# Optimization experiments

Hardware: AMD Instinct MI355X
Metric: run time of the kernel (lower is better)

## Reference

```python
import jax, jax.numpy as jnp
import numpy as np

# Module config (matches init_kwargs)
N_HEADS = 16
HEAD = 64
SEQ = 4096          # single prefill sequence (cu_seqlens_k = [0, SEQ])
BS = 64             # block_size (both q and k blocks)
LOCAL = 8           # local_blocks
VERT = 8            # vert_stride
NB = SEQ // BS      # number of blocks along seq
SLIDE = max(1, VERT // N_HEADS)  # get_head_sliding_step(16, 8, homo_head=False) -> 1
SM_SCALE = 1.0 / float(np.sqrt(HEAD))


def _build_layout():
    """Per-head block-sparse layout: causal + (local OR strided-vertical) blocks,
    padded to a fixed max nnz per row (CSR rows -> padded col indices + valid mask)."""
    h = np.arange(N_HEADS)[:, None, None]
    i = np.arange(NB)[None, :, None]
    j = np.arange(NB)[None, None, :]
    mask = (j <= i) & (((i - j) < LOCAL) | (((j + h * SLIDE + 1) % VERT) == 0))
    max_nnz = int(mask.sum(-1).max())
    cols = np.zeros((N_HEADS, NB, max_nnz), np.int32)
    valid = np.zeros((N_HEADS, NB, max_nnz), bool)
    for hh in range(N_HEADS):
        for ii in range(NB):
            c = np.nonzero(mask[hh, ii])[0]
            cols[hh, ii, :len(c)] = c
            valid[hh, ii, :len(c)] = True
    return cols, valid, max_nnz

_COLS_NP, _VALID_NP, MAX_NNZ = _build_layout()
COLS = jnp.asarray(_COLS_NP)    # [H, NB, NNZ] k-block ids (padded with 0)
VALID = jnp.asarray(_VALID_NP)  # [H, NB, NNZ] padding mask


def setup_inputs() -> dict:
    key = jax.random.key(0)
    kq, kk, kv = jax.random.split(key, 3)
    q = jax.random.normal(kq, (SEQ, N_HEADS, HEAD), jnp.float32)
    k = jax.random.normal(kk, (SEQ, N_HEADS, HEAD), jnp.float32)
    v = jax.random.normal(kv, (SEQ, N_HEADS, HEAD), jnp.float32)
    cu_seqlens_k = jnp.array([0, SEQ], jnp.int32)
    return {"q": q, "k": k, "v": v, "cu_seqlens_k": cu_seqlens_k}


def _attn(q, k, v):
    # [T, H, D] -> [H, NB, BS, D]
    qb = q.transpose(1, 0, 2).reshape(N_HEADS, NB, BS, HEAD)
    kb = k.transpose(1, 0, 2).reshape(N_HEADS, NB, BS, HEAD)
    vb = v.transpose(1, 0, 2).reshape(N_HEADS, NB, BS, HEAD)
    gather = jax.vmap(lambda x, c: x[c])  # per-head block gather
    kg = gather(kb, COLS)  # [H, NB, NNZ, BS, D]
    vg = gather(vb, COLS)  # [H, NB, NNZ, BS, D]
    # block-sparse scores: [H, NB(q blk), BS(m), NNZ(n), BS(j)]
    scores = jnp.einsum('himd,hinjd->himnj', qb, kg) * SM_SCALE
    qpos = jnp.arange(NB)[:, None] * BS + jnp.arange(BS)[None, :]   # [NB, BS]
    kpos = COLS[..., None] * BS + jnp.arange(BS)                    # [H, NB, NNZ, BS]
    allow = VALID[:, :, None, :, None] & (
        qpos[None, :, :, None, None] >= kpos[:, :, None, :, :])
    scores = jnp.where(allow, scores, -jnp.inf)
    p = jax.nn.softmax(scores.reshape(N_HEADS, NB, BS, MAX_NNZ * BS), axis=-1)
    p = p.reshape(N_HEADS, NB, BS, MAX_NNZ, BS)
    out = jnp.einsum('himnj,hinjd->himd', p, vg)
    return out.reshape(N_HEADS, SEQ, HEAD).transpose(1, 0, 2)  # [T, H, D]


def reference(q, k, v, cu_seqlens_k):
    # single-sequence prefill: past_len = 0, q_len == k_len == SEQ
    return _attn(q, k, v)
```

## Files before the change

kernel.cpp:

```cpp
#include <hip/hip_runtime.h>
#include <hip/hip_bf16.h>
#include <math.h>


#define NHEADS 16
#define HDIM   64
#define NBLK   64
#define SEQLEN 4096
#define KP     72
#define SMAX   16.0f

typedef __attribute__((ext_vector_type(8))) short bf16x8;
typedef __attribute__((ext_vector_type(4))) float f32x4;

__device__ __forceinline__ short f2bf(float x) {
    union { float f; unsigned u; } c; c.f = x;
    unsigned u = c.u;
    return (short)((u + 0x7FFFu + ((u >> 16) & 1u)) >> 16);
}

__device__ __forceinline__ void load_lds16(const short* g, const short* l) {
    __builtin_amdgcn_global_load_lds(
        (const __attribute__((address_space(1))) void*)g,
        (__attribute__((address_space(3))) void*)l, 16, 0, 0);
}

__global__ __launch_bounds__(256)
void prep_kernel(const float* __restrict__ k, const float* __restrict__ v,
                 short* __restrict__ kt, short* __restrict__ vt) {
    __shared__ short tile[64 * KP];
    const int b = blockIdx.x;
    const int h = b >> 6, jb = b & 63;
    const int tid = threadIdx.x;

    #pragma unroll
    for (int it = 0; it < 4; ++it) {
        int e = it * 1024 + tid * 4;
        int key = e >> 6, d0 = e & 63;
        float4 f = *(const float4*)(v + ((size_t)(jb * 64 + key) * NHEADS + h) * HDIM + d0);
        tile[(d0 + 0) * KP + key] = f2bf(f.x);
        tile[(d0 + 1) * KP + key] = f2bf(f.y);
        tile[(d0 + 2) * KP + key] = f2bf(f.z);
        tile[(d0 + 3) * KP + key] = f2bf(f.w);
    }
    __syncthreads();
    short* vtile = vt + (size_t)b * 4096;
    #pragma unroll
    for (int ii = 0; ii < 2; ++ii) {
        int idx = ii * 256 + tid;
        int d = idx >> 3, gsw = idx & 7;
        int g = gsw ^ (d & 7);
        bf16x8 val = *(const bf16x8*)&tile[d * KP + g * 8];
        *(bf16x8*)(vtile + (size_t)idx * 8) = val;
    }
    short* ktile = kt + (size_t)b * 4096;
    #pragma unroll
    for (int ii = 0; ii < 2; ++ii) {
        int idx = ii * 256 + tid;
        int r = idx >> 3, g = idx & 7;
        const float* src = k + ((size_t)(jb * 64 + r) * NHEADS + h) * HDIM + g * 8;
        float4 f0 = *(const float4*)src;
        float4 f1 = *(const float4*)(src + 4);
        bf16x8 a;
        a[0]=f2bf(f0.x); a[1]=f2bf(f0.y); a[2]=f2bf(f0.z); a[3]=f2bf(f0.w);
        a[4]=f2bf(f1.x); a[5]=f2bf(f1.y); a[6]=f2bf(f1.z); a[7]=f2bf(f1.w);
        int G = r * 8 + (g ^ (r & 7));
        *(bf16x8*)(ktile + (size_t)G * 8) = a;
    }
}

__global__ __launch_bounds__(256, 4)
void attn_kernel(const short* __restrict__ kt, const short* __restrict__ vt,
                 const float* __restrict__ q, float* __restrict__ out) {
    __shared__ short kv[8192];
    __shared__ short pl[4 * 16 * KP];

    const int b    = blockIdx.x;
    const int h    = ((b & 7) << 1) | ((b >> 3) & 1);
    const int g6   = b >> 4;
    const int qi   = (g6 & 1) ? (63 - (g6 >> 1)) : (g6 >> 1);
    const int tid  = threadIdx.x;
    const int wave = tid >> 6;
    const int lane = tid & 63;
    const int l16  = lane & 15;
    const int quad = lane >> 4;
    const int row0 = qi * 64 + wave * 16;
    short* pw = pl + wave * 16 * KP;

    const float* qrow = q + ((size_t)(row0 + l16) * NHEADS + h) * HDIM;
    bf16x8 a_q[2];
    #pragma unroll
    for (int kk = 0; kk < 2; ++kk) {
        const float* src = qrow + kk * 32 + quad * 8;
        float4 f0 = *(const float4*)(src);
        float4 f1 = *(const float4*)(src + 4);
        bf16x8 a;
        a[0]=f2bf(f0.x); a[1]=f2bf(f0.y); a[2]=f2bf(f0.z); a[3]=f2bf(f0.w);
        a[4]=f2bf(f1.x); a[5]=f2bf(f1.y); a[6]=f2bf(f1.z); a[7]=f2bf(f1.w);
        a_q[kk] = a;
    }

    f32x4 o[4];
    float lsum[4];
    #pragma unroll
    for (int nt = 0; nt < 4; ++nt) { o[nt] = (f32x4){0.f,0.f,0.f,0.f}; lsum[nt] = 0.f; }

    const short* kth = kt + (size_t)(h * 64) * 4096;
    const short* vth = vt + (size_t)(h * 64) * 4096;
    const float kscale = 0.125f * 1.4426950408889634f;

    const int j0  = (7 - h) & 7;
    const int loc = (qi > 7) ? (qi - 7) : 0;
    const int nv  = (j0 < loc) ? ((loc - j0 + 7) >> 3) : 0;
    const int T   = nv + (qi - loc + 1);

    const int sbase = wave * 64;
    const int r7    = l16 & 7;
    const int gk0   = (quad ^ r7) * 8;
    const int gk1   = gk0 ^ 32;
    const int rowb  = l16 * 64;

    for (int t = 0; t < T; ++t) {
        const int jb = (t < nv) ? (j0 + 8 * t) : (loc + (t - nv));
        const short* ktb = kth + (size_t)jb * 4096;
        const short* vtb = vth + (size_t)jb * 4096;

        __syncthreads();
        load_lds16(ktb + (size_t)(sbase + lane) * 8,       &kv[sbase * 8]);
        load_lds16(ktb + (size_t)(256 + sbase + lane) * 8, &kv[(256 + sbase) * 8]);
        load_lds16(vtb + (size_t)(sbase + lane) * 8,       &kv[4096 + sbase * 8]);
        load_lds16(vtb + (size_t)(256 + sbase + lane) * 8, &kv[4096 + (256 + sbase) * 8]);
        __syncthreads();

        f32x4 s[4];
        #pragma unroll
        for (int nt = 0; nt < 4; ++nt) {
            bf16x8 k0 = *(const bf16x8*)&kv[nt * 1024 + rowb + gk0];
            bf16x8 k1 = *(const bf16x8*)&kv[nt * 1024 + rowb + gk1];
            s[nt] = (f32x4){0.f,0.f,0.f,0.f};
            s[nt] = __builtin_amdgcn_mfma_f32_16x16x32_bf16(a_q[0], k0, s[nt], 0, 0, 0);
            s[nt] = __builtin_amdgcn_mfma_f32_16x16x32_bf16(a_q[1], k1, s[nt], 0, 0, 0);
        }

        const bool diag = (jb == qi);
        #pragma unroll
        for (int nt = 0; nt < 4; ++nt)
            #pragma unroll
            for (int r = 0; r < 4; ++r) {
                float raw = s[nt][r];
                if (diag) {
                    int n = nt * 16 + l16;
                    int m = wave * 16 + quad * 4 + r;
                    if (n > m) raw = -INFINITY;
                }
                float pv = exp2f(fmaf(raw, kscale, -SMAX));
                s[nt][r] = pv;
                lsum[r] += pv;
            }

        #pragma unroll
        for (int nt = 0; nt < 4; ++nt)
            #pragma unroll
            for (int r = 0; r < 4; ++r)
                pw[(quad * 4 + r) * KP + nt * 16 + l16] = f2bf(s[nt][r]);
        bf16x8 a_p[2];
        #pragma unroll
        for (int kk = 0; kk < 2; ++kk)
            a_p[kk] = *(const bf16x8*)&pw[l16 * KP + kk * 32 + quad * 8];

        #pragma unroll
        for (int nt = 0; nt < 4; ++nt) {
            bf16x8 v0 = *(const bf16x8*)&kv[4096 + nt * 1024 + rowb + gk0];
            bf16x8 v1 = *(const bf16x8*)&kv[4096 + nt * 1024 + rowb + gk1];
            o[nt] = __builtin_amdgcn_mfma_f32_16x16x32_bf16(a_p[0], v0, o[nt], 0, 0, 0);
            o[nt] = __builtin_amdgcn_mfma_f32_16x16x32_bf16(a_p[1], v1, o[nt], 0, 0, 0);
        }
    }

    #pragma unroll
    for (int r = 0; r < 4; ++r) {
        float tsum = lsum[r];
        #pragma unroll
        for (int off = 1; off < 16; off <<= 1)
            tsum += __shfl_xor(tsum, off);
        float inv = 1.0f / tsum;
        int trow = row0 + quad * 4 + r;
        float* orow = out + ((size_t)trow * NHEADS + h) * HDIM;
        #pragma unroll
        for (int nt = 0; nt < 4; ++nt)
            orow[nt * 16 + l16] = o[nt][r] * inv;
    }
}

extern "C" void kernel_launch(void* const* d_in, const int* in_sizes, int n_in,
                              void* d_out, int out_size, void* d_ws, size_t ws_size,
                              hipStream_t stream) {
    const float* q = (const float*)d_in[0];
    const float* k = (const float*)d_in[1];
    const float* v = (const float*)d_in[2];
    float* out = (float*)d_out;

    const size_t tileBytes = (size_t)NHEADS * NBLK * 4096 * sizeof(short);
    short* kt = (short*)d_ws;
    short* vt = (short*)((char*)d_ws + tileBytes);
    prep_kernel<<<dim3(NHEADS * NBLK), dim3(256), 0, stream>>>(k, v, kt, vt);
    attn_kernel<<<dim3(NHEADS * NBLK), dim3(256), 0, stream>>>(kt, vt, q, out);
}
```

Baseline: 126.8 us.

## Process two query blocks per workgroup with double-buffered K/V prefetch

Each workgroup now handles two adjacent query blocks (each wave owns 32 rows of one block), so the K/V tiles loaded into LDS are shared across both query blocks and the grid halves to 512 workgroups. K/V loads are double-buffered so the next tile is fetched while the current one is computed, and waves skip tiles that are outside their block's sparse pattern. It also switches to the hardware exp2 intrinsic and truncating bf16 conversion for P. The cost is more LDS and registers (occupancy hint lowered to 3) and idle waves on tiles that only the other query block needs.

Result: faster. 120.9 us (-4.7%).

```diff
diff --git a/kernel.cpp b/kernel.cpp
--- a/kernel.cpp
+++ b/kernel.cpp
@@ -17,6 +17,10 @@
     union { float f; unsigned u; } c; c.f = x;
     unsigned u = c.u;
     return (short)((u + 0x7FFFu + ((u >> 16) & 1u)) >> 16);
+}
+__device__ __forceinline__ short f2bf_trunc(float x) {
+    union { float f; unsigned u; } c; c.f = x;
+    return (short)(c.u >> 16);
 }
 
 __device__ __forceinline__ void load_lds16(const short* g, const short* l) {
@@ -69,50 +73,61 @@
     }
 }
 
-__global__ __launch_bounds__(256, 4)
+__global__ __launch_bounds__(256, 3)
 void attn_kernel(const short* __restrict__ kt, const short* __restrict__ vt,
                  const float* __restrict__ q, float* __restrict__ out) {
-    __shared__ short kv[8192];
-    __shared__ short pl[4 * 16 * KP];
+    __shared__ short kv[2 * 8192];
+    __shared__ short pl[4 * 32 * KP];
 
     const int b    = blockIdx.x;
     const int h    = ((b & 7) << 1) | ((b >> 3) & 1);
-    const int g6   = b >> 4;
-    const int qi   = (g6 & 1) ? (63 - (g6 >> 1)) : (g6 >> 1);
+    const int g5   = b >> 4;
+    const int m    = (g5 < 16) ? g5 : (47 - g5);
+    const int q0   = 2 * m, q1 = 2 * m + 1;
     const int tid  = threadIdx.x;
     const int wave = tid >> 6;
     const int lane = tid & 63;
     const int l16  = lane & 15;
     const int quad = lane >> 4;
-    const int row0 = qi * 64 + wave * 16;
-    short* pw = pl + wave * 16 * KP;
-
-    const float* qrow = q + ((size_t)(row0 + l16) * NHEADS + h) * HDIM;
-    bf16x8 a_q[2];
-    #pragma unroll
-    for (int kk = 0; kk < 2; ++kk) {
-        const float* src = qrow + kk * 32 + quad * 8;
-        float4 f0 = *(const float4*)(src);
-        float4 f1 = *(const float4*)(src + 4);
-        bf16x8 a;
-        a[0]=f2bf(f0.x); a[1]=f2bf(f0.y); a[2]=f2bf(f0.z); a[3]=f2bf(f0.w);
-        a[4]=f2bf(f1.x); a[5]=f2bf(f1.y); a[6]=f2bf(f1.z); a[7]=f2bf(f1.w);
-        a_q[kk] = a;
-    }
-
-    f32x4 o[4];
-    float lsum[4];
-    #pragma unroll
-    for (int nt = 0; nt < 4; ++nt) { o[nt] = (f32x4){0.f,0.f,0.f,0.f}; lsum[nt] = 0.f; }
+
+    const int myqi = q0 + (wave >> 1);
+    const int row0 = myqi * 64 + (wave & 1) * 32;
+    short* pw = pl + wave * 32 * KP;
+
+    bf16x8 a_q[2][2];
+    #pragma unroll
+    for (int s = 0; s < 2; ++s) {
+        const float* qrow = q + ((size_t)(row0 + s * 16 + l16) * NHEADS + h) * HDIM;
+        #pragma unroll
+        for (int kk = 0; kk < 2; ++kk) {
+            const float* src = qrow + kk * 32 + quad * 8;
+            float4 f0 = *(const float4*)(src);
+            float4 f1 = *(const float4*)(src + 4);
+            bf16x8 a;
+            a[0]=f2bf(f0.x); a[1]=f2bf(f0.y); a[2]=f2bf(f0.z); a[3]=f2bf(f0.w);
+            a[4]=f2bf(f1.x); a[5]=f2bf(f1.y); a[6]=f2bf(f1.z); a[7]=f2bf(f1.w);
+            a_q[s][kk] = a;
+        }
+    }
+
+    f32x4 o[2][4];
+    float lsum[2][4];
+    #pragma unroll
+    for (int s = 0; s < 2; ++s)
+        #pragma unroll
+        for (int nt = 0; nt < 4; ++nt) {
+            o[s][nt] = (f32x4){0.f,0.f,0.f,0.f};
+            lsum[s][nt] = 0.f;
+        }
 
     const short* kth = kt + (size_t)(h * 64) * 4096;
     const short* vth = vt + (size_t)(h * 64) * 4096;
     const float kscale = 0.125f * 1.4426950408889634f;
 
     const int j0  = (7 - h) & 7;
-    const int loc = (qi > 7) ? (qi - 7) : 0;
-    const int nv  = (j0 < loc) ? ((loc - j0 + 7) >> 3) : 0;
-    const int T   = nv + (qi - loc + 1);
+    const int l0  = (q0 > 7) ? (q0 - 7) : 0;
+    const int nv  = (j0 < l0) ? ((l0 - j0 + 7) >> 3) : 0;
+    const int T   = nv + (q1 - l0 + 1);
 
     const int sbase = wave * 64;
     const int r7    = l16 & 7;
@@ -120,76 +135,110 @@
     const int gk1   = gk0 ^ 32;
     const int rowb  = l16 * 64;
 
-    for (int t = 0; t < T; ++t) {
-        const int jb = (t < nv) ? (j0 + 8 * t) : (loc + (t - nv));
-        const short* ktb = kth + (size_t)jb * 4096;
-        const short* vtb = vth + (size_t)jb * 4096;
-
-        __syncthreads();
+    {
+        const short* ktb = kth + (size_t)((0 < nv) ? j0 : l0) * 4096;
+        const short* vtb = vth + (size_t)((0 < nv) ? j0 : l0) * 4096;
         load_lds16(ktb + (size_t)(sbase + lane) * 8,       &kv[sbase * 8]);
         load_lds16(ktb + (size_t)(256 + sbase + lane) * 8, &kv[(256 + sbase) * 8]);
         load_lds16(vtb + (size_t)(sbase + lane) * 8,       &kv[4096 + sbase * 8]);
         load_lds16(vtb + (size_t)(256 + sbase + lane) * 8, &kv[4096 + (256 + sbase) * 8]);
+    }
+
+    for (int t = 0; t < T; ++t) {
+        const int jb = (t < nv) ? (j0 + 8 * t) : (l0 + (t - nv));
+
         __syncthreads();
 
-        f32x4 s[4];
+        if (t + 1 < T) {
+            const int jn = (t + 1 < nv) ? (j0 + 8 * (t + 1)) : (l0 + (t + 1 - nv));
+            const int bo = ((t + 1) & 1) * 8192;
+            const short* ktb = kth + (size_t)jn * 4096;
+            const short* vtb = vth + (size_t)jn * 4096;
+            load_lds16(ktb + (size_t)(sbase + lane) * 8,       &kv[bo + sbase * 8]);
+            load_lds16(ktb + (size_t)(256 + sbase + lane) * 8, &kv[bo + (256 + sbase) * 8]);
+            load_lds16(vtb + (size_t)(sbase + lane) * 8,       &kv[bo + 4096 + sbase * 8]);
+            load_lds16(vtb + (size_t)(256 + sbase + lane) * 8, &kv[bo + 4096 + (256 + sbase) * 8]);
+        }
+
+        const bool part = (jb <= myqi) &&
+                          (((myqi - jb) < 8) || (((jb + h + 1) & 7) == 0));
+        if (part) {
+            const short* kb = &kv[(t & 1) * 8192];
+            const short* vb = kb + 4096;
+
+            f32x4 s[2][4];
+            #pragma unroll
+            for (int nt = 0; nt < 4; ++nt) {
+                bf16x8 k0 = *(const bf16x8*)&kb[nt * 1024 + rowb + gk0];
+                bf16x8 k1 = *(const bf16x8*)&kb[nt * 1024 + rowb + gk1];
+                s[0][nt] = (f32x4){0.f,0.f,0.f,0.f};
+                s[1][nt] = (f32x4){0.f,0.f,0.f,0.f};
+                s[0][nt] = __builtin_amdgcn_mfma_f32_16x16x32_bf16(a_q[0][0], k0, s[0][nt], 0, 0, 0);
+                s[1][nt] = __builtin_amdgcn_mfma_f32_16x16x32_bf16(a_q[1][0], k0, s[1][nt], 0, 0, 0);
+                s[0][nt] = __builtin_amdgcn_mfma_f32_16x16x32_bf16(a_q[0][1], k1, s[0][nt], 0, 0, 0);
+                s[1][nt] = __builtin_amdgcn_mfma_f32_16x16x32_bf16(a_q[1][1], k1, s[1][nt], 0, 0, 0);
+            }
+
+            const bool diag = (jb == myqi);
+            #pragma unroll
+            for (int s2 = 0; s2 < 2; ++s2)
+                #pragma unroll
+                for (int nt = 0; nt < 4; ++nt)
+                    #pragma unroll
+                    for (int r = 0; r < 4; ++r) {
+                        float raw = s[s2][nt][r];
+                        if (diag) {
+                            int n = nt * 16 + l16;
+                            int mm = (wave & 1) * 32 + s2 * 16 + quad * 4 + r;
+                            if (n > mm) raw = -INFINITY;
+                        }
+                        float pv = __builtin_amdgcn_exp2f(fmaf(raw, kscale, -SMAX));
+                        s[s2][nt][r] = pv;
+                        lsum[s2][r] += pv;
+                    }
+
+            #pragma unroll
+            for (int s2 = 0; s2 < 2; ++s2)
+                #pragma unroll
+                for (int nt = 0; nt < 4; ++nt)
+                    #pragma unroll
+                    for (int r = 0; r < 4; ++r)
+                        pw[(s2 * 16 + quad * 4 + r) * KP + nt * 16 + l16] =
+                            f2bf_trunc(s[s2][nt][r]);
+            bf16x8 a_p[2][2];
+            #pragma unroll
+            for (int s2 = 0; s2 < 2; ++s2)
+                #pragma unroll
+                for (int kk = 0; kk < 2; ++kk)
+                    a_p[s2][kk] = *(const bf16x8*)&pw[(s2 * 16 + l16) * KP + kk * 32 + quad * 8];
+
+            #pragma unroll
+            for (int nt = 0; nt < 4; ++nt) {
+                bf16x8 v0 = *(const bf16x8*)&vb[nt * 1024 + rowb + gk0];
+                bf16x8 v1 = *(const bf16x8*)&vb[nt * 1024 + rowb + gk1];
+                o[0][nt] = __builtin_amdgcn_mfma_f32_16x16x32_bf16(a_p[0][0], v0, o[0][nt], 0, 0, 0);
+                o[1][nt] = __builtin_amdgcn_mfma_f32_16x16x32_bf16(a_p[1][0], v0, o[1][nt], 0, 0, 0);
+                o[0][nt] = __builtin_amdgcn_mfma_f32_16x16x32_bf16(a_p[0][1], v1, o[0][nt], 0, 0, 0);
+                o[1][nt] = __builtin_amdgcn_mfma_f32_16x16x32_bf16(a_p[1][1], v1, o[1][nt], 0, 0, 0);
+            }
+        }
+    }
+
+    #pragma unroll
+    for (int s = 0; s < 2; ++s)
         #pragma unroll
-        for (int nt = 0; nt < 4; ++nt) {
-            bf16x8 k0 = *(const bf16x8*)&kv[nt * 1024 + rowb + gk0];
-            bf16x8 k1 = *(const bf16x8*)&kv[nt * 1024 + rowb + gk1];
-            s[nt] = (f32x4){0.f,0.f,0.f,0.f};
-            s[nt] = __builtin_amdgcn_mfma_f32_16x16x32_bf16(a_q[0], k0, s[nt], 0, 0, 0);
-            s[nt] = __builtin_amdgcn_mfma_f32_16x16x32_bf16(a_q[1], k1, s[nt], 0, 0, 0);
-        }
-
-        const bool diag = (jb == qi);
-        #pragma unroll
-        for (int nt = 0; nt < 4; ++nt)
-            #pragma unroll
-            for (int r = 0; r < 4; ++r) {
-                float raw = s[nt][r];
-                if (diag) {
-                    int n = nt * 16 + l16;
-                    int m = wave * 16 + quad * 4 + r;
-                    if (n > m) raw = -INFINITY;
-                }
-                float pv = exp2f(fmaf(raw, kscale, -SMAX));
-                s[nt][r] = pv;
-                lsum[r] += pv;
-            }
-
-        #pragma unroll
-        for (int nt = 0; nt < 4; ++nt)
-            #pragma unroll
-            for (int r = 0; r < 4; ++r)
-                pw[(quad * 4 + r) * KP + nt * 16 + l16] = f2bf(s[nt][r]);
-        bf16x8 a_p[2];
-        #pragma unroll
-        for (int kk = 0; kk < 2; ++kk)
-            a_p[kk] = *(const bf16x8*)&pw[l16 * KP + kk * 32 + quad * 8];
-
-        #pragma unroll
-        for (int nt = 0; nt < 4; ++nt) {
-            bf16x8 v0 = *(const bf16x8*)&kv[4096 + nt * 1024 + rowb + gk0];
-            bf16x8 v1 = *(const bf16x8*)&kv[4096 + nt * 1024 + rowb + gk1];
-            o[nt] = __builtin_amdgcn_mfma_f32_16x16x32_bf16(a_p[0], v0, o[nt], 0, 0, 0);
-            o[nt] = __builtin_amdgcn_mfma_f32_16x16x32_bf16(a_p[1], v1, o[nt], 0, 0, 0);
-        }
-    }
-
-    #pragma unroll
-    for (int r = 0; r < 4; ++r) {
-        float tsum = lsum[r];
-        #pragma unroll
-        for (int off = 1; off < 16; off <<= 1)
-            tsum += __shfl_xor(tsum, off);
-        float inv = 1.0f / tsum;
-        int trow = row0 + quad * 4 + r;
-        float* orow = out + ((size_t)trow * NHEADS + h) * HDIM;
-        #pragma unroll
-        for (int nt = 0; nt < 4; ++nt)
-            orow[nt * 16 + l16] = o[nt][r] * inv;
-    }
+        for (int r = 0; r < 4; ++r) {
+            float tsum = lsum[s][r];
+            #pragma unroll
+            for (int off = 1; off < 16; off <<= 1)
+                tsum += __shfl_xor(tsum, off);
+            float inv = 1.0f / tsum;
+            int trow = row0 + s * 16 + quad * 4 + r;
+            float* orow = out + ((size_t)trow * NHEADS + h) * HDIM;
+            #pragma unroll
+            for (int nt = 0; nt < 4; ++nt)
+                orow[nt * 16 + l16] = o[s][nt][r] * inv;
+        }
 }
 
 extern "C" void kernel_launch(void* const* d_in, const int* in_sizes, int n_in,
@@ -204,5 +253,5 @@
     short* kt = (short*)d_ws;
     short* vt = (short*)((char*)d_ws + tileBytes);
     prep_kernel<<<dim3(NHEADS * NBLK), dim3(256), 0, stream>>>(k, v, kt, vt);
-    attn_kernel<<<dim3(NHEADS * NBLK), dim3(256), 0, stream>>>(kt, vt, q, out);
-}
+    attn_kernel<<<dim3(512), dim3(256), 0, stream>>>(kt, vt, q, out);
+}
```

## Process two query blocks per workgroup with double-buffered K/V loads

Applied to the files above, without the earlier changes.

Each 512-thread workgroup now handles two adjacent query blocks of one head, so the K/V tiles of their shared key blocks are loaded into LDS once and reused by both halves. K/V loads are double-buffered, with the next tile prefetched while the current one is computed, which removes one barrier per iteration. The P tile now uses a swizzled layout with truncating bf16 conversion and the hardware exp2 builtin. Waves whose query block does not use the current key block skip that tile, which costs some wave imbalance, and workgroups are paired light/heavy to balance load across the 512 blocks.

New measurement: 118.4 us. 1.07x faster.

```diff
diff --git a/kernel.cpp b/kernel.cpp
--- a/kernel.cpp
+++ b/kernel.cpp
@@ -17,6 +17,10 @@
     union { float f; unsigned u; } c; c.f = x;
     unsigned u = c.u;
     return (short)((u + 0x7FFFu + ((u >> 16) & 1u)) >> 16);
+}
+__device__ __forceinline__ short f2bf_trunc(float x) {
+    union { float f; unsigned u; } c; c.f = x;
+    return (short)(c.u >> 16);
 }
 
 __device__ __forceinline__ void load_lds16(const short* g, const short* l) {
@@ -69,23 +73,27 @@
     }
 }
 
-__global__ __launch_bounds__(256, 4)
+__global__ __launch_bounds__(512, 4)
 void attn_kernel(const short* __restrict__ kt, const short* __restrict__ vt,
                  const float* __restrict__ q, float* __restrict__ out) {
-    __shared__ short kv[8192];
-    __shared__ short pl[4 * 16 * KP];
+    __shared__ short kv[2 * 8192];
+    __shared__ short pl[8 * 1024];
 
     const int b    = blockIdx.x;
     const int h    = ((b & 7) << 1) | ((b >> 3) & 1);
-    const int g6   = b >> 4;
-    const int qi   = (g6 & 1) ? (63 - (g6 >> 1)) : (g6 >> 1);
+    const int g5   = b >> 4;
+    const int m    = (g5 < 16) ? g5 : (47 - g5);
+    const int q0   = 2 * m, q1 = 2 * m + 1;
     const int tid  = threadIdx.x;
     const int wave = tid >> 6;
     const int lane = tid & 63;
     const int l16  = lane & 15;
     const int quad = lane >> 4;
-    const int row0 = qi * 64 + wave * 16;
-    short* pw = pl + wave * 16 * KP;
+
+    const int myqi   = q0 + (wave >> 2);
+    const int stripe = wave & 3;
+    const int row0   = myqi * 64 + stripe * 16;
+    short* pw = pl + wave * 1024;
 
     const float* qrow = q + ((size_t)(row0 + l16) * NHEADS + h) * HDIM;
     bf16x8 a_q[2];
@@ -110,70 +118,84 @@
     const float kscale = 0.125f * 1.4426950408889634f;
 
     const int j0  = (7 - h) & 7;
-    const int loc = (qi > 7) ? (qi - 7) : 0;
-    const int nv  = (j0 < loc) ? ((loc - j0 + 7) >> 3) : 0;
-    const int T   = nv + (qi - loc + 1);
-
-    const int sbase = wave * 64;
-    const int r7    = l16 & 7;
-    const int gk0   = (quad ^ r7) * 8;
-    const int gk1   = gk0 ^ 32;
-    const int rowb  = l16 * 64;
+    const int l0  = (q0 > 7) ? (q0 - 7) : 0;
+    const int nv  = (j0 < l0) ? ((l0 - j0 + 7) >> 3) : 0;
+    const int T   = nv + (q1 - l0 + 1);
+
+    const int r7   = l16 & 7;
+    const int gk0  = (quad ^ r7) * 8;
+    const int gk1  = gk0 ^ 32;
+    const int rowb = l16 * 64;
+    const int pr0  = rowb + (((  quad) ^ r7) << 3);
+    const int pr1  = rowb + (((4 + quad) ^ r7) << 3);
+
+    {
+        const short* ktb = kth + (size_t)((0 < nv) ? j0 : l0) * 4096;
+        const short* vtb = vth + (size_t)((0 < nv) ? j0 : l0) * 4096;
+        load_lds16(ktb + (size_t)tid * 8, &kv[wave * 512]);
+        load_lds16(vtb + (size_t)tid * 8, &kv[4096 + wave * 512]);
+    }
 
     for (int t = 0; t < T; ++t) {
-        const int jb = (t < nv) ? (j0 + 8 * t) : (loc + (t - nv));
-        const short* ktb = kth + (size_t)jb * 4096;
-        const short* vtb = vth + (size_t)jb * 4096;
+        const int jb = (t < nv) ? (j0 + 8 * t) : (l0 + (t - nv));
 
         __syncthreads();
-        load_lds16(ktb + (size_t)(sbase + lane) * 8,       &kv[sbase * 8]);
-        load_lds16(ktb + (size_t)(256 + sbase + lane) * 8, &kv[(256 + sbase) * 8]);
-        load_lds16(vtb + (size_t)(sbase + lane) * 8,       &kv[4096 + sbase * 8]);
-        load_lds16(vtb + (size_t)(256 + sbase + lane) * 8, &kv[4096 + (256 + sbase) * 8]);
-        __syncthreads();
-
-        f32x4 s[4];
-        #pragma unroll
-        for (int nt = 0; nt < 4; ++nt) {
-            bf16x8 k0 = *(const bf16x8*)&kv[nt * 1024 + rowb + gk0];
-            bf16x8 k1 = *(const bf16x8*)&kv[nt * 1024 + rowb + gk1];
-            s[nt] = (f32x4){0.f,0.f,0.f,0.f};
-            s[nt] = __builtin_amdgcn_mfma_f32_16x16x32_bf16(a_q[0], k0, s[nt], 0, 0, 0);
-            s[nt] = __builtin_amdgcn_mfma_f32_16x16x32_bf16(a_q[1], k1, s[nt], 0, 0, 0);
+
+        if (t + 1 < T) {
+            const int jn = (t + 1 < nv) ? (j0 + 8 * (t + 1)) : (l0 + (t + 1 - nv));
+            const int bo = ((t + 1) & 1) * 8192;
+            const short* ktb = kth + (size_t)jn * 4096;
+            const short* vtb = vth + (size_t)jn * 4096;
+            load_lds16(ktb + (size_t)tid * 8, &kv[bo + wave * 512]);
+            load_lds16(vtb + (size_t)tid * 8, &kv[bo + 4096 + wave * 512]);
         }
 
-        const bool diag = (jb == qi);
-        #pragma unroll
-        for (int nt = 0; nt < 4; ++nt)
+        const bool part = (jb <= myqi) &&
+                          (((myqi - jb) < 8) || (((jb + h + 1) & 7) == 0));
+        if (part) {
+            const short* kb = &kv[(t & 1) * 8192];
+            const short* vb = kb + 4096;
+
+            f32x4 s[4];
             #pragma unroll
-            for (int r = 0; r < 4; ++r) {
-                float raw = s[nt][r];
-                if (diag) {
-                    int n = nt * 16 + l16;
-                    int m = wave * 16 + quad * 4 + r;
-                    if (n > m) raw = -INFINITY;
+            for (int nt = 0; nt < 4; ++nt) {
+                bf16x8 k0 = *(const bf16x8*)&kb[nt * 1024 + rowb + gk0];
+                bf16x8 k1 = *(const bf16x8*)&kb[nt * 1024 + rowb + gk1];
+                s[nt] = (f32x4){0.f,0.f,0.f,0.f};
+                s[nt] = __builtin_amdgcn_mfma_f32_16x16x32_bf16(a_q[0], k0, s[nt], 0, 0, 0);
+                s[nt] = __builtin_amdgcn_mfma_f32_16x16x32_bf16(a_q[1], k1, s[nt], 0, 0, 0);
+            }
+
+            const bool diag = (jb == myqi);
+            #pragma unroll
+            for (int nt = 0; nt < 4; ++nt) {
+                const int gw = nt * 2 + (l16 >> 3);
+                const int ow = l16 & 7;
+                #pragma unroll
+                for (int r = 0; r < 4; ++r) {
+                    float raw = s[nt][r];
+                    const int mrow = stripe * 16 + quad * 4 + r;
+                    if (diag) {
+                        int n = nt * 16 + l16;
+                        if (n > mrow) raw = -INFINITY;
+                    }
+                    float pv = __builtin_amdgcn_exp2f(fmaf(raw, kscale, -SMAX));
+                    lsum[r] += pv;
+                    const int prow = quad * 4 + r;
+                    pw[prow * 64 + ((gw ^ (prow & 7)) << 3) + ow] = f2bf_trunc(pv);
                 }
-                float pv = exp2f(fmaf(raw, kscale, -SMAX));
-                s[nt][r] = pv;
-                lsum[r] += pv;
             }
 
-        #pragma unroll
-        for (int nt = 0; nt < 4; ++nt)
+            bf16x8 a_p0 = *(const bf16x8*)&pw[pr0];
+            bf16x8 a_p1 = *(const bf16x8*)&pw[pr1];
+
             #pragma unroll
-            for (int r = 0; r < 4; ++r)
-                pw[(quad * 4 + r) * KP + nt * 16 + l16] = f2bf(s[nt][r]);
-        bf16x8 a_p[2];
-        #pragma unroll
-        for (int kk = 0; kk < 2; ++kk)
-            a_p[kk] = *(const bf16x8*)&pw[l16 * KP + kk * 32 + quad * 8];
-
-        #pragma unroll
-        for (int nt = 0; nt < 4; ++nt) {
-            bf16x8 v0 = *(const bf16x8*)&kv[4096 + nt * 1024 + rowb + gk0];
-            bf16x8 v1 = *(const bf16x8*)&kv[4096 + nt * 1024 + rowb + gk1];
-            o[nt] = __builtin_amdgcn_mfma_f32_16x16x32_bf16(a_p[0], v0, o[nt], 0, 0, 0);
-            o[nt] = __builtin_amdgcn_mfma_f32_16x16x32_bf16(a_p[1], v1, o[nt], 0, 0, 0);
+            for (int nt = 0; nt < 4; ++nt) {
+                bf16x8 v0 = *(const bf16x8*)&vb[nt * 1024 + rowb + gk0];
+                bf16x8 v1 = *(const bf16x8*)&vb[nt * 1024 + rowb + gk1];
+                o[nt] = __builtin_amdgcn_mfma_f32_16x16x32_bf16(a_p0, v0, o[nt], 0, 0, 0);
+                o[nt] = __builtin_amdgcn_mfma_f32_16x16x32_bf16(a_p1, v1, o[nt], 0, 0, 0);
+            }
         }
     }
 
@@ -204,5 +226,5 @@
     short* kt = (short*)d_ws;
     short* vt = (short*)((char*)d_ws + tileBytes);
     prep_kernel<<<dim3(NHEADS * NBLK), dim3(256), 0, stream>>>(k, v, kt, vt);
-    attn_kernel<<<dim3(NHEADS * NBLK), dim3(256), 0, stream>>>(kt, vt, q, out);
-}
+    attn_kernel<<<dim3(512), dim3(512), 0, stream>>>(kt, vt, q, out);
+}
```
